# Performance work log

Hardware: AMD Instinct MI355X
Metric: run time of the kernel (lower is better)

## Reference

```python
import jax, jax.numpy as jnp
import numpy as np

HASH_PRIME = 5099  # primes[layer_id=0]
MIN_CAPACITY = 4


def setup_inputs() -> dict:
    key = jax.random.key(0)
    k1, k2, k3, k4, k5 = jax.random.split(key, 5)
    B, T, D, F, E = 8, 4096, 512, 1792, 64
    x = jax.random.normal(k1, (B, T, D), dtype=jnp.float32)
    token_ids = jax.random.randint(k2, (B, T), 0, 50257, dtype=jnp.int32)
    # Expert params stacked over E (random instead of the degenerate zero init)
    Wk = jax.random.normal(k3, (E, F, D), dtype=jnp.float32) * 0.02
    Wr = jax.random.normal(k4, (E, D, D), dtype=jnp.float32) * 0.02
    Wv = jax.random.normal(k5, (E, D, F), dtype=jnp.float32) * 0.02
    return {"x": x, "token_ids": token_ids, "Wk": Wk, "Wr": Wr, "Wv": Wv}


def reference(x, token_ids, Wk, Wr, Wv):
    B, T, D = x.shape
    E = Wk.shape[0]
    S = B * T
    # capacity_factor = 1, k = 1 -> capacity = ceil(S / E), at least min_capacity
    cap = max(MIN_CAPACITY, -(-S // E))

    tid = token_ids.reshape(S)
    e_idx = (tid % HASH_PRIME) % E                     # hash routing, top-1, gate weight 1.0

    onehot = jax.nn.one_hot(e_idx, E, dtype=jnp.int32)  # [S, E]
    rank = (jnp.cumsum(onehot, axis=0) * onehot).sum(axis=1)  # 1-based rank within expert
    pos = rank - 1                                      # slot index within expert
    kept = pos < cap                                    # capacity drop (first-come order)

    xf = x.reshape(S, D)
    pos_safe = jnp.where(kept, pos, cap)                # out-of-bounds -> dropped by scatter
    dispatched = jnp.zeros((E, cap, D), x.dtype).at[e_idx, pos_safe].set(xf, mode='drop')

    # RWKV expert FFN, batched over experts
    h = jnp.square(jax.nn.relu(jnp.einsum('ecd,efd->ecf', dispatched, Wk)))  # [E,C,F]
    kv = jnp.einsum('ecf,edf->ecd', h, Wv)                                   # [E,C,D]
    r = jax.nn.sigmoid(jnp.einsum('ecd,egd->ecg', dispatched, Wr))           # [E,C,D]
    expert_out = r * kv

    # combine: gather each token's slot; dropped tokens get zeros
    yf = expert_out[e_idx, jnp.minimum(pos, cap - 1)] * kept[:, None].astype(x.dtype)
    return yf.reshape(B, T, D)
```

## Files before the change

kernel.cpp:

```cpp
#include <hip/hip_runtime.h>
#include <hip/hip_fp16.h>

#define HASH_PRIME 5099
#define NE 64
#define ND 512
#define NF 1792
#define NS 32768
#define CAP 512

typedef unsigned short u16;
typedef __attribute__((ext_vector_type(8))) short bf16x8;
typedef __attribute__((ext_vector_type(4))) float f32x4;

__device__ __forceinline__ u16 f2bf(float f) {
  union { float f; unsigned u; } v; v.f = f;
  return (u16)((v.u + 0x7FFFu + ((v.u >> 16) & 1u)) >> 16);
}
__device__ __forceinline__ unsigned pkbf2(float a, float b) {
  return (unsigned)f2bf(a) | ((unsigned)f2bf(b) << 16);
}

__device__ __forceinline__ void gld16(const void* g, void* l) {
  __builtin_amdgcn_global_load_lds(
      (const __attribute__((address_space(1))) unsigned int*)(uintptr_t)g,
      (__attribute__((address_space(3))) unsigned int*)(uintptr_t)l,
      16, 0, 0);
}

__global__ __launch_bounds__(512) void route1(const int* __restrict__ tok,
                                              int* __restrict__ rank_local,
                                              int* __restrict__ hist) {
  __shared__ int se[512];
  __shared__ int h[NE];
  int b = blockIdx.x, t = threadIdx.x;
  int s = b * 512 + t;
  int e = (tok[s] % HASH_PRIME) % NE;
  se[t] = e;
  if (t < NE) h[t] = 0;
  __syncthreads();
  int cnt = 0;
  for (int j = 0; j < t; ++j) cnt += (se[j] == e);
  rank_local[s] = cnt;
  atomicAdd(&h[e], 1);
  __syncthreads();
  if (t < NE) hist[b * NE + t] = h[t];
}

__global__ __launch_bounds__(512) void route2(const int* __restrict__ tok,
                                              const int* __restrict__ rank_local,
                                              const int* __restrict__ hist,
                                              int* __restrict__ slot_src) {
  __shared__ int off[NE];
  int b = blockIdx.x, t = threadIdx.x;
  if (t < NE) {
    int o = 0;
    for (int bb = 0; bb < b; ++bb) o += hist[bb * NE + t];
    off[t] = o;
  }
  __syncthreads();
  int s = b * 512 + t;
  int e = (tok[s] % HASH_PRIME) % NE;
  int pos = off[e] + rank_local[s];
  if (pos < CAP) slot_src[e * CAP + pos] = s;
}

__global__ __launch_bounds__(256) void dispatchx(const float* __restrict__ x,
                                                 const int* __restrict__ slot_src,
                                                 u16* __restrict__ Xd) {
  int b = blockIdx.x;
  int t = threadIdx.x;
  int row = b * 4 + (t >> 6);
  int col = (t & 63) * 8;
  int s = slot_src[row];
  uint4 w = make_uint4(0u, 0u, 0u, 0u);
  if (s >= 0) {
    const float4* p = (const float4*)(x + (size_t)s * ND + col);
    float4 a = p[0], c = p[1];
    w.x = pkbf2(a.x, a.y); w.y = pkbf2(a.z, a.w);
    w.z = pkbf2(c.x, c.y); w.w = pkbf2(c.z, c.w);
  }
  *(uint4*)(Xd + (size_t)row * ND + col) = w;
}


#define GDECL \
  __shared__ u16 As[2][256 * 32]; \
  __shared__ u16 Bs[2][128 * 32]; \
  const int t = threadIdx.x; \
  const int l = t & 63; \
  const int w = t >> 6; \
  const int wm = w >> 1; \
  const int wn = w & 1; \
  const int lrow = l & 15; \
  const int kb = l >> 4; \
  const int brow = t >> 2; \
  const int bseg = t & 3;

#define INIT_ACC do { \
  _Pragma("unroll") for (int m_ = 0; m_ < 4; ++m_) \
    _Pragma("unroll") for (int n_ = 0; n_ < 4; ++n_) \
      acc[m_][n_] = (f32x4){0.f, 0.f, 0.f, 0.f}; \
} while (0)

#define ISSUE_A(buf, ks, abase, astride) do { \
  const u16* g_ = (abase) + (size_t)(w * 32 + (l >> 2)) * (astride) + (ks) * 32 + (l & 3) * 8; \
  gld16(g_, (char*)&As[buf][0] + w * 2048); \
  gld16(g_ + (size_t)16 * (astride), (char*)&As[buf][0] + w * 2048 + 1024); \
} while (0)

#define LOAD_B(ks, bbase, bstride) do { \
  const float4* p_ = (const float4*)((bbase) + (size_t)brow * (bstride) + (ks) * 32 + bseg * 8); \
  fb0 = p_[0]; fb1 = p_[1]; \
} while (0)

#define WRITE_B(buf) do { \
  uint4 wv_; \
  wv_.x = pkbf2(fb0.x, fb0.y); wv_.y = pkbf2(fb0.z, fb0.w); \
  wv_.z = pkbf2(fb1.x, fb1.y); wv_.w = pkbf2(fb1.z, fb1.w); \
  *(uint4*)&Bs[buf][brow * 32 + bseg * 8] = wv_; \
} while (0)

#define COMPUTE(buf) do { \
  bf16x8 af_[4], bf_[4]; \
  _Pragma("unroll") for (int m_ = 0; m_ < 4; ++m_) \
    af_[m_] = *(const bf16x8*)&As[buf][(wm * 64 + m_ * 16 + lrow) * 32 + kb * 8]; \
  _Pragma("unroll") for (int n_ = 0; n_ < 4; ++n_) \
    bf_[n_] = *(const bf16x8*)&Bs[buf][(wn * 64 + n_ * 16 + lrow) * 32 + kb * 8]; \
  _Pragma("unroll") for (int m_ = 0; m_ < 4; ++m_) \
    _Pragma("unroll") for (int n_ = 0; n_ < 4; ++n_) \
      acc[m_][n_] = __builtin_amdgcn_mfma_f32_16x16x32_bf16(af_[m_], bf_[n_], acc[m_][n_], 0, 0, 0); \
} while (0)

#define GEMM_LOOP(NK, abase, astride, bbase, bstride) do { \
  float4 fb0, fb1; \
  ISSUE_A(0, 0, abase, astride); \
  LOAD_B(0, bbase, bstride); \
  WRITE_B(0); \
  __syncthreads(); \
  _Pragma("unroll 2") \
  for (int ks = 0; ks < (NK); ++ks) { \
    const int cur = ks & 1; \
    if (ks + 1 < (NK)) { \
      ISSUE_A(cur ^ 1, ks + 1, abase, astride); \
      LOAD_B(ks + 1, bbase, bstride); \
    } \
    COMPUTE(cur); \
    if (ks + 1 < (NK)) WRITE_B(cur ^ 1); \
    __syncthreads(); \
  } \
} while (0)

__global__ __launch_bounds__(512, 4) void g1(const u16* __restrict__ Xd,
                                             const float* __restrict__ Wk,
                                             u16* __restrict__ H) {
  GDECL
  const int wg = (blockIdx.x & 7) * (1792 / 8) + (blockIdx.x >> 3);
  const int e = wg / 28, rem = wg % 28;
  const int n0 = (rem >> 1) * 128;
  const int m0 = (rem & 1) * 256;
  f32x4 acc[4][4];
  INIT_ACC;
  const u16*  abase = Xd + ((size_t)e * CAP + m0) * ND;
  const float* bbase = Wk + ((size_t)e * NF + n0) * ND;
  GEMM_LOOP(16, abase, ND, bbase, ND);

  #pragma unroll
  for (int m = 0; m < 4; ++m) {
    #pragma unroll
    for (int i = 0; i < 4; ++i) {
      int r = m0 + wm * 64 + m * 16 + (l >> 4) * 4 + i;
      size_t base = ((size_t)e * CAP + r) * NF + n0 + wn * 64 + lrow;
      #pragma unroll
      for (int n = 0; n < 4; ++n) {
        float v = acc[m][n][i];
        v = v > 0.f ? v * v : 0.f;
        H[base + n * 16] = f2bf(v);
      }
    }
  }
}

__global__ __launch_bounds__(512, 4) void g2a(const u16* __restrict__ Xd,
                                              const float* __restrict__ Wr,
                                              __half* __restrict__ R) {
  GDECL
  const int wg = (blockIdx.x & 7) * (512 / 8) + (blockIdx.x >> 3);
  const int e = wg / 8, rem = wg % 8;
  const int n0 = (rem >> 1) * 128;
  const int m0 = (rem & 1) * 256;
  f32x4 acc[4][4];
  INIT_ACC;
  const u16*  abase = Xd + ((size_t)e * CAP + m0) * ND;
  const float* bbase = Wr + ((size_t)e * ND + n0) * ND;
  GEMM_LOOP(16, abase, ND, bbase, ND);

  #pragma unroll
  for (int m = 0; m < 4; ++m) {
    #pragma unroll
    for (int i = 0; i < 4; ++i) {
      int r = m0 + wm * 64 + m * 16 + (l >> 4) * 4 + i;
      size_t base = ((size_t)e * CAP + r) * ND + n0 + wn * 64 + lrow;
      #pragma unroll
      for (int n = 0; n < 4; ++n) {
        float s = 1.f / (1.f + __expf(-acc[m][n][i]));
        R[base + n * 16] = __float2half(s);
      }
    }
  }
}

__global__ __launch_bounds__(512, 4) void g2b(const u16* __restrict__ H,
                                              const float* __restrict__ Wv,
                                              const __half* __restrict__ R,
                                              const int* __restrict__ slot_src,
                                              float* __restrict__ out) {
  GDECL
  __shared__ int ss[256];
  const int wg = (blockIdx.x & 7) * (512 / 8) + (blockIdx.x >> 3);
  const int e = wg / 8, rem = wg % 8;
  const int n0 = (rem >> 1) * 128;
  const int m0 = (rem & 1) * 256;
  if (t < 256) ss[t] = slot_src[e * CAP + m0 + t];
  f32x4 acc[4][4];
  INIT_ACC;
  const u16*  abase = H  + ((size_t)e * CAP + m0) * NF;
  const float* bbase = Wv + ((size_t)e * ND + n0) * NF;
  GEMM_LOOP(56, abase, NF, bbase, NF);

  #pragma unroll
  for (int m = 0; m < 4; ++m) {
    #pragma unroll
    for (int i = 0; i < 4; ++i) {
      int rl = wm * 64 + m * 16 + (l >> 4) * 4 + i;
      int s = ss[rl];
      if (s >= 0) {
        const __half* rp = R + ((size_t)e * CAP + m0 + rl) * ND + n0 + wn * 64 + lrow;
        float* op = out + (size_t)s * ND + n0 + wn * 64 + lrow;
        #pragma unroll
        for (int n = 0; n < 4; ++n) {
          op[n * 16] = __half2float(rp[n * 16]) * acc[m][n][i];
        }
      }
    }
  }
}

extern "C" void kernel_launch(void* const* d_in, const int* in_sizes, int n_in,
                              void* d_out, int out_size, void* d_ws, size_t ws_size,
                              hipStream_t stream) {
  const float* x   = (const float*)d_in[0];
  const int*   tok = (const int*)d_in[1];
  const float* Wk  = (const float*)d_in[2];
  const float* Wr  = (const float*)d_in[3];
  const float* Wv  = (const float*)d_in[4];
  float* out = (float*)d_out;

  char* ws = (char*)d_ws;
  int*    slot_src   = (int*)ws;
  int*    rank_local = (int*)(ws + 131072);
  int*    hist       = (int*)(ws + 262144);
  u16*    Xd         = (u16*)(ws + (1 << 20));
  __half* R          = (__half*)(ws + 34603008);
  u16*    H          = (u16*)(ws + 68157440);

  (void)hipMemsetAsync(d_out, 0, (size_t)out_size * sizeof(float), stream);
  (void)hipMemsetAsync(slot_src, 0xFF, NE * CAP * sizeof(int), stream);
  route1<<<64, 512, 0, stream>>>(tok, rank_local, hist);
  route2<<<64, 512, 0, stream>>>(tok, rank_local, hist, slot_src);
  dispatchx<<<NS / 4, 256, 0, stream>>>(x, slot_src, Xd);
  g1 <<<1792, 512, 0, stream>>>(Xd, Wk, H);
  g2a<<<512,  512, 0, stream>>>(Xd, Wr, R);
  g2b<<<512,  512, 0, stream>>>(H, Wv, R, slot_src, out);
}
```

Before: 343.4 us.

## Restructure expert GEMMs into 256x256 tiles with swizzled LDS and phased pipeline

Replaces the 256x128 double-buffered GEMM loop with a 256x256 output tile per block, a BK=64 K-step, and XOR-swizzled LDS layouts for A and B. Each K iteration is split into four phases that interleave global loads, fp32-to-bf16 conversion of B, LDS reads and MFMA bursts, using explicit barriers, waitcnts and s_setprio. The aim is higher arithmetic intensity per byte loaded, fewer LDS bank conflicts, and better overlap of memory and compute. The cost is twice as many accumulators, occupancy lowered to 2 blocks per CU, and fewer blocks launched, which may underfill the GPU. g2b now reads slot_src from global memory instead of staging it in shared memory.

```diff
diff --git a/kernel.cpp b/kernel.cpp
--- a/kernel.cpp
+++ b/kernel.cpp
@@ -84,91 +84,150 @@
 
 
 #define GDECL \
-  __shared__ u16 As[2][256 * 32]; \
-  __shared__ u16 Bs[2][128 * 32]; \
+  __shared__ u16 AsH[2 * 256 * 64]; \
+  __shared__ u16 BsH[2 * 256 * 64]; \
   const int t = threadIdx.x; \
   const int l = t & 63; \
   const int w = t >> 6; \
-  const int wm = w >> 1; \
-  const int wn = w & 1; \
+  const int wm = w >> 2; \
+  const int wn = w & 3; \
   const int lrow = l & 15; \
   const int kb = l >> 4; \
-  const int brow = t >> 2; \
-  const int bseg = t & 3;
-
-#define INIT_ACC do { \
-  _Pragma("unroll") for (int m_ = 0; m_ < 4; ++m_) \
+  const int rsw0_ = ((kb) ^ (l & 7)) * 8; \
+  const int rsw1_ = ((4 + kb) ^ (l & 7)) * 8; \
+  const int arow_ = w * 8 + (l >> 3); \
+  const int asw_ = ((l & 7) ^ (l >> 3)) * 8; \
+  const int brow_ = (t >> 7) * 64 + ((t >> 2) & 31); \
+  const int bkq_ = t & 3; \
+  const int bsa_ = ((bkq_ * 2) ^ (brow_ & 7)) * 8; \
+  const int bsb_ = ((bkq_ * 2 + 1) ^ (brow_ & 7)) * 8;
+
+#define GLDA(sl, rbase, ktS, abase, AST) do { \
+  const u16* g_ = (abase) + (size_t)((rbase) + arow_) * (AST) + (size_t)(ktS) * 64 + asw_; \
+  gld16(g_, (char*)AsH + (sl) * 32768 + (rbase) * 128 + t * 16); \
+} while (0)
+
+#define LOADB(dst, ktS, u, bbase, BST) do { \
+  const float4* p_ = (const float4*)((bbase) + (size_t)(brow_ + (u) * 32) * (BST) + (size_t)(ktS) * 64 + bkq_ * 16); \
+  dst[0] = p_[0]; dst[1] = p_[1]; dst[2] = p_[2]; dst[3] = p_[3]; \
+} while (0)
+
+#define WRB(sl, u, src) do { \
+  uint4 w0_, w1_; \
+  w0_.x = pkbf2(src[0].x, src[0].y); w0_.y = pkbf2(src[0].z, src[0].w); \
+  w0_.z = pkbf2(src[1].x, src[1].y); w0_.w = pkbf2(src[1].z, src[1].w); \
+  w1_.x = pkbf2(src[2].x, src[2].y); w1_.y = pkbf2(src[2].z, src[2].w); \
+  w1_.z = pkbf2(src[3].x, src[3].y); w1_.w = pkbf2(src[3].z, src[3].w); \
+  *(uint4*)&BsH[(sl) * 16384 + (brow_ + (u) * 32) * 64 + bsa_] = w0_; \
+  *(uint4*)&BsH[(sl) * 16384 + (brow_ + (u) * 32) * 64 + bsb_] = w1_; \
+} while (0)
+
+#define RDA(mh, slotH) do { \
+  _Pragma("unroll") for (int ml_ = 0; ml_ < 4; ++ml_) { \
+    const int r_ = wm * 128 + ((mh) * 4 + ml_) * 16 + lrow; \
+    af[ml_][0] = *(const bf16x8*)&AsH[(slotH) + r_ * 64 + rsw0_]; \
+    af[ml_][1] = *(const bf16x8*)&AsH[(slotH) + r_ * 64 + rsw1_]; \
+  } \
+} while (0)
+
+#define RDB(np, slotH) do { \
+  _Pragma("unroll") for (int nl_ = 0; nl_ < 2; ++nl_) { \
+    const int r_ = wn * 64 + ((np) * 2 + nl_) * 16 + lrow; \
+    bf[nl_][0] = *(const bf16x8*)&BsH[(slotH) + r_ * 64 + rsw0_]; \
+    bf[nl_][1] = *(const bf16x8*)&BsH[(slotH) + r_ * 64 + rsw1_]; \
+  } \
+} while (0)
+
+#define MFMA16(mh, np) do { \
+  _Pragma("unroll") for (int ml_ = 0; ml_ < 4; ++ml_) \
+    _Pragma("unroll") for (int nl_ = 0; nl_ < 2; ++nl_) \
+      _Pragma("unroll") for (int ks_ = 0; ks_ < 2; ++ks_) \
+        acc[(mh) * 4 + ml_][(np) * 2 + nl_] = __builtin_amdgcn_mfma_f32_16x16x32_bf16( \
+            af[ml_][ks_], bf[nl_][ks_], acc[(mh) * 4 + ml_][(np) * 2 + nl_], 0, 0, 0); \
+} while (0)
+
+#define FENCE() asm volatile("" ::: "memory")
+#define BAR()  do { FENCE(); __builtin_amdgcn_s_barrier(); FENCE(); } while (0)
+#define LGKM0() asm volatile("s_waitcnt lgkmcnt(0)" ::: "memory")
+#define VMW(n) asm volatile("s_waitcnt vmcnt(" #n ")" ::: "memory")
+
+#define GEMM_CORE(NKT, abase, AST, bbase, BST) \
+  f32x4 acc[8][4]; \
+  _Pragma("unroll") for (int m_ = 0; m_ < 8; ++m_) \
     _Pragma("unroll") for (int n_ = 0; n_ < 4; ++n_) \
       acc[m_][n_] = (f32x4){0.f, 0.f, 0.f, 0.f}; \
-} while (0)
-
-#define ISSUE_A(buf, ks, abase, astride) do { \
-  const u16* g_ = (abase) + (size_t)(w * 32 + (l >> 2)) * (astride) + (ks) * 32 + (l & 3) * 8; \
-  gld16(g_, (char*)&As[buf][0] + w * 2048); \
-  gld16(g_ + (size_t)16 * (astride), (char*)&As[buf][0] + w * 2048 + 1024); \
-} while (0)
-
-#define LOAD_B(ks, bbase, bstride) do { \
-  const float4* p_ = (const float4*)((bbase) + (size_t)brow * (bstride) + (ks) * 32 + bseg * 8); \
-  fb0 = p_[0]; fb1 = p_[1]; \
-} while (0)
-
-#define WRITE_B(buf) do { \
-  uint4 wv_; \
-  wv_.x = pkbf2(fb0.x, fb0.y); wv_.y = pkbf2(fb0.z, fb0.w); \
-  wv_.z = pkbf2(fb1.x, fb1.y); wv_.w = pkbf2(fb1.z, fb1.w); \
-  *(uint4*)&Bs[buf][brow * 32 + bseg * 8] = wv_; \
-} while (0)
-
-#define COMPUTE(buf) do { \
-  bf16x8 af_[4], bf_[4]; \
-  _Pragma("unroll") for (int m_ = 0; m_ < 4; ++m_) \
-    af_[m_] = *(const bf16x8*)&As[buf][(wm * 64 + m_ * 16 + lrow) * 32 + kb * 8]; \
-  _Pragma("unroll") for (int n_ = 0; n_ < 4; ++n_) \
-    bf_[n_] = *(const bf16x8*)&Bs[buf][(wn * 64 + n_ * 16 + lrow) * 32 + kb * 8]; \
-  _Pragma("unroll") for (int m_ = 0; m_ < 4; ++m_) \
-    _Pragma("unroll") for (int n_ = 0; n_ < 4; ++n_) \
-      acc[m_][n_] = __builtin_amdgcn_mfma_f32_16x16x32_bf16(af_[m_], bf_[n_], acc[m_][n_], 0, 0, 0); \
-} while (0)
-
-#define GEMM_LOOP(NK, abase, astride, bbase, bstride) do { \
-  float4 fb0, fb1; \
-  ISSUE_A(0, 0, abase, astride); \
-  LOAD_B(0, bbase, bstride); \
-  WRITE_B(0); \
-  __syncthreads(); \
+  bf16x8 af[4][2]; \
+  float4 fq[4], fu1[4]; \
+   \
+  GLDA(0, 0, 0, abase, AST); GLDA(0, 128, 0, abase, AST); \
+  GLDA(0, 64, 0, abase, AST); GLDA(0, 192, 0, abase, AST); \
+  LOADB(fq, 0, 0, bbase, BST); \
+  LOADB(fu1, 0, 1, bbase, BST); \
+  WRB(0, 0, fq); \
+  VMW(0); \
+  LGKM0(); \
+  BAR(); \
   _Pragma("unroll 2") \
-  for (int ks = 0; ks < (NK); ++ks) { \
-    const int cur = ks & 1; \
-    if (ks + 1 < (NK)) { \
-      ISSUE_A(cur ^ 1, ks + 1, abase, astride); \
-      LOAD_B(ks + 1, bbase, bstride); \
+  for (int kt = 0; kt < (NKT); ++kt) { \
+    const int slot = kt & 1, ss_ = slot ^ 1; \
+    const int slotH = slot * 16384; \
+    const int ktS = (kt + 1 < (NKT)) ? kt + 1 : 0; \
+    {  \
+      bf16x8 bf[2][2]; \
+      RDA(0, slotH); RDB(0, slotH); \
+      GLDA(ss_, 0, ktS, abase, AST); GLDA(ss_, 128, ktS, abase, AST); \
+      WRB(slot, 1, fu1);  \
+      BAR(); LGKM0(); \
+      __builtin_amdgcn_s_setprio(1); MFMA16(0, 0); __builtin_amdgcn_s_setprio(0); \
+      BAR(); \
     } \
-    COMPUTE(cur); \
-    if (ks + 1 < (NK)) WRITE_B(cur ^ 1); \
-    __syncthreads(); \
+    {  \
+      bf16x8 bf[2][2]; \
+      RDB(1, slotH); \
+      LOADB(fq, ktS, 0, bbase, BST); \
+      BAR(); LGKM0(); \
+      __builtin_amdgcn_s_setprio(1); MFMA16(0, 1); __builtin_amdgcn_s_setprio(0); \
+      VMW(6);   \
+      BAR(); \
+    } \
+    {  \
+      bf16x8 bf[2][2]; \
+      RDA(1, slotH); RDB(0, slotH); \
+      LOADB(fu1, ktS, 1, bbase, BST); \
+      BAR(); LGKM0(); \
+      __builtin_amdgcn_s_setprio(1); MFMA16(1, 0); __builtin_amdgcn_s_setprio(0); \
+      BAR(); \
+    } \
+    {  \
+      bf16x8 bf[2][2]; \
+      RDB(1, slotH); \
+      GLDA(ss_, 64, ktS, abase, AST); GLDA(ss_, 192, ktS, abase, AST); \
+      WRB(ss_, 0, fq);  \
+      BAR(); LGKM0(); \
+      __builtin_amdgcn_s_setprio(1); MFMA16(1, 1); __builtin_amdgcn_s_setprio(0); \
+      VMW(10);  \
+      BAR(); \
+    } \
   } \
-} while (0)
-
-__global__ __launch_bounds__(512, 4) void g1(const u16* __restrict__ Xd,
+  VMW(0);
+
+__global__ __launch_bounds__(512, 2) void g1(const u16* __restrict__ Xd,
                                              const float* __restrict__ Wk,
                                              u16* __restrict__ H) {
   GDECL
-  const int wg = (blockIdx.x & 7) * (1792 / 8) + (blockIdx.x >> 3);
-  const int e = wg / 28, rem = wg % 28;
-  const int n0 = (rem >> 1) * 128;
+  const int wg = (blockIdx.x & 7) * 112 + (blockIdx.x >> 3);
+  const int e = wg / 14, rem = wg % 14;
   const int m0 = (rem & 1) * 256;
-  f32x4 acc[4][4];
-  INIT_ACC;
+  const int n0 = (rem >> 1) * 256;
   const u16*  abase = Xd + ((size_t)e * CAP + m0) * ND;
   const float* bbase = Wk + ((size_t)e * NF + n0) * ND;
-  GEMM_LOOP(16, abase, ND, bbase, ND);
+  GEMM_CORE(8, abase, ND, bbase, ND)
 
   #pragma unroll
-  for (int m = 0; m < 4; ++m) {
+  for (int m = 0; m < 8; ++m) {
     #pragma unroll
     for (int i = 0; i < 4; ++i) {
-      int r = m0 + wm * 64 + m * 16 + (l >> 4) * 4 + i;
+      int r = m0 + wm * 128 + m * 16 + (l >> 4) * 4 + i;
       size_t base = ((size_t)e * CAP + r) * NF + n0 + wn * 64 + lrow;
       #pragma unroll
       for (int n = 0; n < 4; ++n) {
@@ -180,25 +239,23 @@
   }
 }
 
-__global__ __launch_bounds__(512, 4) void g2a(const u16* __restrict__ Xd,
+__global__ __launch_bounds__(512, 2) void g2a(const u16* __restrict__ Xd,
                                               const float* __restrict__ Wr,
                                               __half* __restrict__ R) {
   GDECL
-  const int wg = (blockIdx.x & 7) * (512 / 8) + (blockIdx.x >> 3);
-  const int e = wg / 8, rem = wg % 8;
-  const int n0 = (rem >> 1) * 128;
+  const int wg = (blockIdx.x & 7) * 32 + (blockIdx.x >> 3);
+  const int e = wg >> 2, rem = wg & 3;
   const int m0 = (rem & 1) * 256;
-  f32x4 acc[4][4];
-  INIT_ACC;
+  const int n0 = (rem >> 1) * 256;
   const u16*  abase = Xd + ((size_t)e * CAP + m0) * ND;
   const float* bbase = Wr + ((size_t)e * ND + n0) * ND;
-  GEMM_LOOP(16, abase, ND, bbase, ND);
+  GEMM_CORE(8, abase, ND, bbase, ND)
 
   #pragma unroll
-  for (int m = 0; m < 4; ++m) {
+  for (int m = 0; m < 8; ++m) {
     #pragma unroll
     for (int i = 0; i < 4; ++i) {
-      int r = m0 + wm * 64 + m * 16 + (l >> 4) * 4 + i;
+      int r = m0 + wm * 128 + m * 16 + (l >> 4) * 4 + i;
       size_t base = ((size_t)e * CAP + r) * ND + n0 + wn * 64 + lrow;
       #pragma unroll
       for (int n = 0; n < 4; ++n) {
@@ -209,32 +266,28 @@
   }
 }
 
-__global__ __launch_bounds__(512, 4) void g2b(const u16* __restrict__ H,
+__global__ __launch_bounds__(512, 2) void g2b(const u16* __restrict__ H,
                                               const float* __restrict__ Wv,
                                               const __half* __restrict__ R,
                                               const int* __restrict__ slot_src,
                                               float* __restrict__ out) {
   GDECL
-  __shared__ int ss[256];
-  const int wg = (blockIdx.x & 7) * (512 / 8) + (blockIdx.x >> 3);
-  const int e = wg / 8, rem = wg % 8;
-  const int n0 = (rem >> 1) * 128;
+  const int wg = (blockIdx.x & 7) * 32 + (blockIdx.x >> 3);
+  const int e = wg >> 2, rem = wg & 3;
   const int m0 = (rem & 1) * 256;
-  if (t < 256) ss[t] = slot_src[e * CAP + m0 + t];
-  f32x4 acc[4][4];
-  INIT_ACC;
+  const int n0 = (rem >> 1) * 256;
   const u16*  abase = H  + ((size_t)e * CAP + m0) * NF;
   const float* bbase = Wv + ((size_t)e * ND + n0) * NF;
-  GEMM_LOOP(56, abase, NF, bbase, NF);
+  GEMM_CORE(28, abase, NF, bbase, NF)
 
   #pragma unroll
-  for (int m = 0; m < 4; ++m) {
+  for (int m = 0; m < 8; ++m) {
     #pragma unroll
     for (int i = 0; i < 4; ++i) {
-      int rl = wm * 64 + m * 16 + (l >> 4) * 4 + i;
-      int s = ss[rl];
+      int rl = m0 + wm * 128 + m * 16 + (l >> 4) * 4 + i;
+      int s = slot_src[e * CAP + rl];
       if (s >= 0) {
-        const __half* rp = R + ((size_t)e * CAP + m0 + rl) * ND + n0 + wn * 64 + lrow;
+        const __half* rp = R + ((size_t)e * CAP + rl) * ND + n0 + wn * 64 + lrow;
         float* op = out + (size_t)s * ND + n0 + wn * 64 + lrow;
         #pragma unroll
         for (int n = 0; n < 4; ++n) {
@@ -261,14 +314,14 @@
   int*    hist       = (int*)(ws + 262144);
   u16*    Xd         = (u16*)(ws + (1 << 20));
   __half* R          = (__half*)(ws + 34603008);
-  u16*    H          = (u16*)(ws + 68157440);
+  u16*    Hbuf       = (u16*)(ws + 68157440);
 
   (void)hipMemsetAsync(d_out, 0, (size_t)out_size * sizeof(float), stream);
   (void)hipMemsetAsync(slot_src, 0xFF, NE * CAP * sizeof(int), stream);
   route1<<<64, 512, 0, stream>>>(tok, rank_local, hist);
   route2<<<64, 512, 0, stream>>>(tok, rank_local, hist, slot_src);
   dispatchx<<<NS / 4, 256, 0, stream>>>(x, slot_src, Xd);
-  g1 <<<1792, 512, 0, stream>>>(Xd, Wk, H);
-  g2a<<<512,  512, 0, stream>>>(Xd, Wr, R);
-  g2b<<<512,  512, 0, stream>>>(H, Wv, R, slot_src, out);
-}
+  g1 <<<896, 512, 0, stream>>>(Xd, Wk, Hbuf);
+  g2a<<<256, 512, 0, stream>>>(Xd, Wr, R);
+  g2b<<<256, 512, 0, stream>>>(Hbuf, Wv, R, slot_src, out);
+}
```

After: 383.1 us. +11.5%, slower.
